# Kernel optimization log

Measured on AMD Instinct MI355X. Metric: run time of the kernel, lower is better.

The kernel has to match this reference:

```python
import jax, jax.numpy as jnp
import numpy as np

IN_FEATURES = 128
HIDDEN_DIM = 128
ALPHA = 0.2
NEG_INF = -9e15


def setup_inputs() -> dict:
    key = jax.random.key(0)
    k1, k2, k3, k4, k5 = jax.random.split(key, 5)
    N, n_context = 20000, 32
    h_i = jax.random.normal(k1, (N, IN_FEATURES), dtype=jnp.float32)
    context_indices = jax.random.randint(k2, (N, n_context), 0, N, dtype=jnp.int64)
    # learned params (torch nn.Linear default init scale ~ U(-1/sqrt(fan_in), 1/sqrt(fan_in)))
    s1 = 1.0 / np.sqrt(IN_FEATURES)
    s2 = 1.0 / np.sqrt(2 * HIDDEN_DIM)
    W_i = jax.random.uniform(k3, (IN_FEATURES, HIDDEN_DIM), jnp.float32, -s1, s1)
    W_j = jax.random.uniform(k4, (IN_FEATURES, HIDDEN_DIM), jnp.float32, -s1, s1)
    ka, kb = jax.random.split(k5)
    a_w = jax.random.uniform(ka, (2 * HIDDEN_DIM, 1), jnp.float32, -s2, s2)
    a_b = jax.random.uniform(kb, (1,), jnp.float32, -s2, s2)
    return {"h_i": h_i, "context_indices": context_indices,
            "W_i": W_i, "W_j": W_j, "a_w": a_w, "a_b": a_b}


def reference(h_i, context_indices, W_i, W_j, a_w, a_b):
    N, n_context = context_indices.shape
    # -1 padding maps to an extra zero row (torch indexes -1 -> last row of padded table)
    h_padded = jnp.concatenate([h_i, jnp.zeros((1, h_i.shape[1]), h_i.dtype)], axis=0)
    idx = jnp.where(context_indices >= 0, context_indices, N)
    h_j = h_padded[idx]                      # [N, n_context, in_features]
    Wh_i = h_i @ W_i                         # [N, hidden]
    Wh_j = jnp.einsum('ncf,fh->nch', h_j, W_j)  # [N, n_context, hidden]
    # attention_layer(cat(Wh_i, Wh_j)) split into two matvecs (same math as concat)
    a_i, a_j = a_w[:HIDDEN_DIM, 0], a_w[HIDDEN_DIM:, 0]
    e = Wh_i @ a_i                           # [N]
    e = e[:, None] + Wh_j @ a_j + a_b[0]     # [N, n_context]
    e = jax.nn.leaky_relu(e, ALPHA)
    e = jnp.where(context_indices >= 0, e, NEG_INF)
    attn = jax.nn.softmax(e, axis=1)         # [N, n_context]
    h_prime = jnp.einsum('nc,nch->nh', attn, Wh_j)
    return h_prime
```

## Files before the change

kernel.cpp:

```cpp
#include <hip/hip_runtime.h>
#include <hip/hip_fp16.h>

#define GAT_ALPHA 0.2f
#define GAT_NEG_INF -9.0e15f

typedef _Float16 half8_t __attribute__((ext_vector_type(8)));
typedef float f32x4 __attribute__((ext_vector_type(4)));

__global__ __launch_bounds__(256) void gat_transform_mfma(
    const float* __restrict__ h, const float* __restrict__ Wi,
    const float* __restrict__ Wj, const float* __restrict__ aw,
    const float* __restrict__ ab,
    __half* __restrict__ Wh16, float* __restrict__ e1, float* __restrict__ e2,
    int N) {
    __shared__ _Float16 sWt[128 * 136];
    __shared__ float svi[128];
    const int t = threadIdx.x;

    if (t < 128) {
        const float4* wrow = (const float4*)(Wi + (size_t)t * 128);
        const float4* a4 = (const float4*)aw;
        float s = 0.f;
        #pragma unroll
        for (int i = 0; i < 32; ++i) {
            float4 w = wrow[i], a = a4[i];
            s = fmaf(w.x, a.x, s); s = fmaf(w.y, a.y, s);
            s = fmaf(w.z, a.z, s); s = fmaf(w.w, a.w, s);
        }
        svi[t] = s;
    }
    for (int i = t; i < 128 * 128; i += 256) {
        int k = i >> 7, n = i & 127;
        sWt[n * 136 + k] = (_Float16)Wj[i];
    }
    __syncthreads();

    const int wave = t >> 6, lane = t & 63, q = lane >> 4, l16 = lane & 15;
    const float abv = ab[0];

    float vir[4][8];
    #pragma unroll
    for (int s = 0; s < 4; ++s) {
        float4 u0 = *(const float4*)(svi + s * 32 + q * 8);
        float4 u1 = *(const float4*)(svi + s * 32 + q * 8 + 4);
        vir[s][0] = u0.x; vir[s][1] = u0.y; vir[s][2] = u0.z; vir[s][3] = u0.w;
        vir[s][4] = u1.x; vir[s][5] = u1.y; vir[s][6] = u1.z; vir[s][7] = u1.w;
    }
    float ajr[8];
    #pragma unroll
    for (int c = 0; c < 8; ++c) ajr[c] = aw[128 + c * 16 + l16];

    const int ntiles = (N + 15) >> 4;
    for (int tile = blockIdx.x * 4 + wave; tile < ntiles; tile += gridDim.x * 4) {
        const int base = tile << 4;
        int row = base + l16; if (row >= N) row = N - 1;
        const float* hp = h + (size_t)row * 128 + q * 8;

        half8_t af[4];
        float pe1 = 0.f;
        #pragma unroll
        for (int s = 0; s < 4; ++s) {
            float4 f0 = *(const float4*)(hp + s * 32);
            float4 f1 = *(const float4*)(hp + s * 32 + 4);
            pe1 = fmaf(f0.x, vir[s][0], pe1); pe1 = fmaf(f0.y, vir[s][1], pe1);
            pe1 = fmaf(f0.z, vir[s][2], pe1); pe1 = fmaf(f0.w, vir[s][3], pe1);
            pe1 = fmaf(f1.x, vir[s][4], pe1); pe1 = fmaf(f1.y, vir[s][5], pe1);
            pe1 = fmaf(f1.z, vir[s][6], pe1); pe1 = fmaf(f1.w, vir[s][7], pe1);
            half8_t a;
            a[0] = (_Float16)f0.x; a[1] = (_Float16)f0.y;
            a[2] = (_Float16)f0.z; a[3] = (_Float16)f0.w;
            a[4] = (_Float16)f1.x; a[5] = (_Float16)f1.y;
            a[6] = (_Float16)f1.z; a[7] = (_Float16)f1.w;
            af[s] = a;
        }

        f32x4 acc[8];
        #pragma unroll
        for (int c = 0; c < 8; ++c) { f32x4 z = {0.f, 0.f, 0.f, 0.f}; acc[c] = z; }

        const _Float16* wbase = sWt + l16 * 136 + q * 8;
        #pragma unroll
        for (int s = 0; s < 4; ++s) {
            #pragma unroll
            for (int c = 0; c < 8; ++c) {
                half8_t bf = *(const half8_t*)(wbase + c * (16 * 136) + s * 32);
                acc[c] = __builtin_amdgcn_mfma_f32_16x16x32_f16(af[s], bf, acc[c], 0, 0, 0);
            }
        }

        const bool full = (base + 16 <= N);
        float pe2[4] = {0.f, 0.f, 0.f, 0.f};
        #pragma unroll
        for (int c = 0; c < 8; ++c) {
            #pragma unroll
            for (int r = 0; r < 4; ++r) {
                float v = acc[c][r];
                pe2[r] = fmaf(v, ajr[c], pe2[r]);
                int rr = base + q * 4 + r;
                if (full || rr < N)
                    Wh16[(size_t)rr * 128 + (c * 16 + l16)] = __float2half(v);
            }
        }
        #pragma unroll
        for (int r = 0; r < 4; ++r) {
            pe2[r] += __shfl_xor(pe2[r], 1);
            pe2[r] += __shfl_xor(pe2[r], 2);
            pe2[r] += __shfl_xor(pe2[r], 4);
            pe2[r] += __shfl_xor(pe2[r], 8);
        }
        if (l16 == 0) {
            #pragma unroll
            for (int r = 0; r < 4; ++r) {
                int rr = base + q * 4 + r;
                if (rr < N) e2[rr] = pe2[r];
            }
        }
        pe1 += __shfl_xor(pe1, 16);
        pe1 += __shfl_xor(pe1, 32);
        if (lane < 16) {
            int rr = base + lane;
            if (rr < N) e1[rr] = pe1 + abv;
        }
    }
}

__global__ __launch_bounds__(256) void gat_gather4(
    const int* __restrict__ ctx, const float* __restrict__ e1,
    const float* __restrict__ e2, const __half* __restrict__ Wh16,
    float* __restrict__ out, int N) {
    const int t = threadIdx.x;
    const int wave = t >> 6, lane = t & 63, qid = lane >> 4, l = lane & 15;
    const int widx = blockIdx.x * 4 + wave;
    if (widx * 4 >= N) return;
    const int n = widx * 4 + qid;
    const bool okn = (n < N);
    const int nn = okn ? n : (N - 1);

    int2 ij = ((const int2*)(ctx + (size_t)nn * 32))[l];
    const bool v0 = (ij.x >= 0), v1 = (ij.y >= 0);
    const int j0 = v0 ? ij.x : 0, j1 = v1 ? ij.y : 0;
    const float eb = e1[nn];
    float lg0 = eb + e2[j0], lg1 = eb + e2[j1];
    lg0 = fmaxf(lg0, GAT_ALPHA * lg0);
    lg1 = fmaxf(lg1, GAT_ALPHA * lg1);
    lg0 = v0 ? lg0 : GAT_NEG_INF;
    lg1 = v1 ? lg1 : GAT_NEG_INF;
    float m = fmaxf(lg0, lg1);
    #pragma unroll
    for (int s = 8; s; s >>= 1) m = fmaxf(m, __shfl_xor(m, s, 16));
    float p0 = v0 ? __expf(lg0 - m) : 0.f;
    float p1 = v1 ? __expf(lg1 - m) : 0.f;
    float ss = p0 + p1;
    #pragma unroll
    for (int s = 8; s; s >>= 1) ss += __shfl_xor(ss, s, 16);
    const float inv = (ss > 0.f) ? __frcp_rn(ss) : 0.f;
    p0 *= inv; p1 *= inv;

    const int o0 = j0 << 8, o1 = j1 << 8;
    float a0 = 0.f, a1 = 0.f, a2 = 0.f, a3 = 0.f;
    float a4 = 0.f, a5 = 0.f, a6 = 0.f, a7 = 0.f;
    const char* wb = (const char*)Wh16 + (size_t)(l * 16);
    #pragma unroll 8
    for (int cc = 0; cc < 32; ++cc) {
        const int src = cc >> 1;
        float w   = __shfl((cc & 1) ? p1 : p0, src, 16);
        int   off = __shfl((cc & 1) ? o1 : o0, src, 16);
        half8_t hv = *(const half8_t*)(wb + off);
        a0 = fmaf(w, (float)hv[0], a0); a1 = fmaf(w, (float)hv[1], a1);
        a2 = fmaf(w, (float)hv[2], a2); a3 = fmaf(w, (float)hv[3], a3);
        a4 = fmaf(w, (float)hv[4], a4); a5 = fmaf(w, (float)hv[5], a5);
        a6 = fmaf(w, (float)hv[6], a6); a7 = fmaf(w, (float)hv[7], a7);
    }
    if (okn) {
        float4* orow = (float4*)(out + (size_t)n * 128);
        float4 u; u.x = a0; u.y = a1; u.z = a2; u.w = a3;
        float4 v; v.x = a4; v.y = a5; v.z = a6; v.w = a7;
        orow[2 * l] = u;
        orow[2 * l + 1] = v;
    }
}

extern "C" void kernel_launch(void* const* d_in, const int* in_sizes, int n_in,
                              void* d_out, int out_size, void* d_ws, size_t ws_size,
                              hipStream_t stream) {
    const float* h   = (const float*)d_in[0];
    const int*   ctx = (const int*)d_in[1];
    const float* Wi  = (const float*)d_in[2];
    const float* Wj  = (const float*)d_in[3];
    const float* aw  = (const float*)d_in[4];
    const float* ab  = (const float*)d_in[5];
    float* out = (float*)d_out;
    const int N = in_sizes[0] / 128;

    float* e1 = (float*)d_ws;
    float* e2 = e1 + N;
    __half* Wh16 = (__half*)(e2 + N);

    const int ntiles = (N + 15) >> 4;
    const int g1 = (ntiles + 3) / 4;
    const int nquad = (N + 3) / 4;
    const int g2 = (nquad + 3) / 4;

    gat_transform_mfma<<<g1, 256, 0, stream>>>(h, Wi, Wj, aw, ab, Wh16, e1, e2, N);
    gat_gather4<<<g2, 256, 0, stream>>>(ctx, e1, e2, Wh16, out, N);
}
```

Measured before the change: 101.7 us.

## Assign one wave per node in gather kernel with cross-quarter reduction

```diff
diff --git a/kernel.cpp b/kernel.cpp
--- a/kernel.cpp
+++ b/kernel.cpp
@@ -124,59 +124,64 @@
     }
 }
 
-__global__ __launch_bounds__(256) void gat_gather4(
+__global__ __launch_bounds__(256, 8) void gat_gather1(
     const int* __restrict__ ctx, const float* __restrict__ e1,
     const float* __restrict__ e2, const __half* __restrict__ Wh16,
     float* __restrict__ out, int N) {
     const int t = threadIdx.x;
-    const int wave = t >> 6, lane = t & 63, qid = lane >> 4, l = lane & 15;
-    const int widx = blockIdx.x * 4 + wave;
-    if (widx * 4 >= N) return;
-    const int n = widx * 4 + qid;
-    const bool okn = (n < N);
-    const int nn = okn ? n : (N - 1);
-
-    int2 ij = ((const int2*)(ctx + (size_t)nn * 32))[l];
-    const bool v0 = (ij.x >= 0), v1 = (ij.y >= 0);
-    const int j0 = v0 ? ij.x : 0, j1 = v1 ? ij.y : 0;
-    const float eb = e1[nn];
-    float lg0 = eb + e2[j0], lg1 = eb + e2[j1];
-    lg0 = fmaxf(lg0, GAT_ALPHA * lg0);
-    lg1 = fmaxf(lg1, GAT_ALPHA * lg1);
-    lg0 = v0 ? lg0 : GAT_NEG_INF;
-    lg1 = v1 ? lg1 : GAT_NEG_INF;
-    float m = fmaxf(lg0, lg1);
-    #pragma unroll
-    for (int s = 8; s; s >>= 1) m = fmaxf(m, __shfl_xor(m, s, 16));
-    float p0 = v0 ? __expf(lg0 - m) : 0.f;
-    float p1 = v1 ? __expf(lg1 - m) : 0.f;
-    float ss = p0 + p1;
-    #pragma unroll
-    for (int s = 8; s; s >>= 1) ss += __shfl_xor(ss, s, 16);
+    const int wave = t >> 6, lane = t & 63;
+    const int qq = lane >> 4, ll = lane & 15;
+    const int n = blockIdx.x * 4 + wave;
+    if (n >= N) return;
+
+    const int c32 = lane & 31;
+    const int j = ctx[(size_t)n * 32 + c32];
+    const bool v = (j >= 0);
+    const int jj = v ? j : 0;
+    const float eb = e1[n];
+    float lg = eb + e2[jj];
+    lg = fmaxf(lg, GAT_ALPHA * lg);
+    lg = v ? lg : GAT_NEG_INF;
+    float m = lg;
+    #pragma unroll
+    for (int s = 16; s; s >>= 1) m = fmaxf(m, __shfl_xor(m, s, 32));
+    float p = v ? __expf(lg - m) : 0.f;
+    float ss = p;
+    #pragma unroll
+    for (int s = 16; s; s >>= 1) ss += __shfl_xor(ss, s, 32);
     const float inv = (ss > 0.f) ? __frcp_rn(ss) : 0.f;
-    p0 *= inv; p1 *= inv;
-
-    const int o0 = j0 << 8, o1 = j1 << 8;
+    p *= inv;
+    const int o = jj << 8;
+
     float a0 = 0.f, a1 = 0.f, a2 = 0.f, a3 = 0.f;
     float a4 = 0.f, a5 = 0.f, a6 = 0.f, a7 = 0.f;
-    const char* wb = (const char*)Wh16 + (size_t)(l * 16);
-    #pragma unroll 8
-    for (int cc = 0; cc < 32; ++cc) {
-        const int src = cc >> 1;
-        float w   = __shfl((cc & 1) ? p1 : p0, src, 16);
-        int   off = __shfl((cc & 1) ? o1 : o0, src, 16);
+    const char* wb = (const char*)Wh16 + (size_t)(ll * 16);
+    #pragma unroll
+    for (int k = 0; k < 8; ++k) {
+        const int src = qq * 8 + k;
+        const float w = __shfl(p, src, 32);
+        const int  off = __shfl(o, src, 32);
         half8_t hv = *(const half8_t*)(wb + off);
         a0 = fmaf(w, (float)hv[0], a0); a1 = fmaf(w, (float)hv[1], a1);
         a2 = fmaf(w, (float)hv[2], a2); a3 = fmaf(w, (float)hv[3], a3);
         a4 = fmaf(w, (float)hv[4], a4); a5 = fmaf(w, (float)hv[5], a5);
         a6 = fmaf(w, (float)hv[6], a6); a7 = fmaf(w, (float)hv[7], a7);
     }
-    if (okn) {
+    a0 += __shfl_xor(a0, 16); a1 += __shfl_xor(a1, 16);
+    a2 += __shfl_xor(a2, 16); a3 += __shfl_xor(a3, 16);
+    a4 += __shfl_xor(a4, 16); a5 += __shfl_xor(a5, 16);
+    a6 += __shfl_xor(a6, 16); a7 += __shfl_xor(a7, 16);
+    a0 += __shfl_xor(a0, 32); a1 += __shfl_xor(a1, 32);
+    a2 += __shfl_xor(a2, 32); a3 += __shfl_xor(a3, 32);
+    a4 += __shfl_xor(a4, 32); a5 += __shfl_xor(a5, 32);
+    a6 += __shfl_xor(a6, 32); a7 += __shfl_xor(a7, 32);
+
+    if (lane < 16) {
         float4* orow = (float4*)(out + (size_t)n * 128);
         float4 u; u.x = a0; u.y = a1; u.z = a2; u.w = a3;
-        float4 v; v.x = a4; v.y = a5; v.z = a6; v.w = a7;
-        orow[2 * l] = u;
-        orow[2 * l + 1] = v;
+        float4 w2; w2.x = a4; w2.y = a5; w2.z = a6; w2.w = a7;
+        orow[2 * ll] = u;
+        orow[2 * ll + 1] = w2;
     }
 }
 
@@ -198,9 +203,8 @@
 
     const int ntiles = (N + 15) >> 4;
     const int g1 = (ntiles + 3) / 4;
-    const int nquad = (N + 3) / 4;
-    const int g2 = (nquad + 3) / 4;
+    const int g2 = (N + 3) / 4;
 
     gat_transform_mfma<<<g1, 256, 0, stream>>>(h, Wi, Wj, aw, ab, Wh16, e1, e2, N);
-    gat_gather4<<<g2, 256, 0, stream>>>(ctx, e1, e2, Wh16, out, N);
+    gat_gather1<<<g2, 256, 0, stream>>>(ctx, e1, e2, Wh16, out, N);
 }
```

Result: no change. 102.3 us (+0.6%).
